# Performance work log

Measured on AMD Instinct MI355X. Metric: run time of the kernel, lower is better.

Reference implementation:

```python
import jax, jax.numpy as jnp
import numpy as np

N_NODES = 50000
N_EDGES = 1_600_000
NFEAT, NHID, NLAYERS, NCLASS = 512, 256, 4, 40


def spmm(edge_src, edge_dst, edge_val, X):
    # sparse adj (COO) @ X : gather rows by src, scale, scatter-add to dst
    msg = X[edge_src] * edge_val[:, None]          # [E, F]
    return jax.ops.segment_sum(msg, edge_dst, num_segments=N_NODES)


def setup_inputs() -> dict:
    key = jax.random.key(0)
    ks = jax.random.split(key, 16)
    x = jax.random.normal(ks[0], (N_NODES, NFEAT), dtype=jnp.float32)
    edge_src = jax.random.randint(ks[1], (N_EDGES,), 0, N_NODES, dtype=jnp.int32)
    edge_dst = jax.random.randint(ks[2], (N_EDGES,), 0, N_NODES, dtype=jnp.int32)
    edge_val = jax.random.uniform(ks[3], (N_EDGES,), dtype=jnp.float32)

    def mk_w(k, fan_in, fan_out):
        return jax.random.normal(k, (fan_in, fan_out), dtype=jnp.float32) / jnp.sqrt(jnp.float32(fan_in))

    inp = {"x": x, "edge_val": edge_val, "edge_src": edge_src, "edge_dst": edge_dst}
    for k in range(NLAYERS):
        fan_in = k * NHID + NFEAT
        inp[f"W{k}"] = mk_w(ks[4 + k], fan_in, NHID)
        inp[f"b{k}"] = jnp.zeros((NHID,), dtype=jnp.float32)
    inp["W_out"] = mk_w(ks[12], NLAYERS * NHID + NFEAT, NCLASS)
    inp["b_out"] = jnp.zeros((NCLASS,), dtype=jnp.float32)
    return inp


def reference(x, edge_val, W0, b0, W1, b1, W2, b2, W3, b3, W_out, b_out, edge_src, edge_dst):
    Ws = [(W0, b0), (W1, b1), (W2, b2), (W3, b3)]
    blocks = [x]
    for W, b in Ws:
        h = jnp.concatenate(blocks, axis=1)                       # [N, k*nhid+nfeat]
        h = spmm(edge_src, edge_dst, edge_val, h @ W) + b          # snowball_layer
        blocks.append(jnp.tanh(h))                                 # dropout no-op (eval)
    h = jnp.concatenate(blocks, axis=1)                            # [N, nlayers*nhid+nfeat]
    out = spmm(edge_src, edge_dst, edge_val, h @ W_out) + b_out    # out layer, eye=False
    return jax.nn.log_softmax(out, axis=1)
```

## Files before the change

### kernel.cpp

```cpp
#include <hip/hip_runtime.h>
#include <hip/hip_bf16.h>
#include <math.h>

#define N_NODES 50000
#define N_EDGES 1600000
#define NFEAT   512
#define NHID    256
#define NCLASS  40
#define HCOLS   1536

typedef __attribute__((ext_vector_type(8))) short bf16x8s;
typedef __attribute__((ext_vector_type(4))) float f32x4;

__device__ __forceinline__ ushort f2bf(float f) {
    uint u = __builtin_bit_cast(uint, f);
    uint r = (u + 0x7fffu + ((u >> 16) & 1u)) >> 16;
    return (ushort)r;
}
__device__ __forceinline__ float bf2f(ushort u) {
    uint t = (uint)u << 16;
    return __builtin_bit_cast(float, t);
}

__global__ __launch_bounds__(256) void copy_x_bf16_kernel(const float4* __restrict__ x4,
                                                          ushort* __restrict__ Hb) {
    const int total = N_NODES * (NFEAT / 4);
    for (int idx = blockIdx.x * blockDim.x + threadIdx.x; idx < total;
         idx += gridDim.x * blockDim.x) {
        int node = idx >> 7;
        int j    = idx & 127;
        float4 v = x4[idx];
        ushort4 o;
        o.x = f2bf(v.x); o.y = f2bf(v.y); o.z = f2bf(v.z); o.w = f2bf(v.w);
        *(ushort4*)&Hb[(size_t)node * HCOLS + j * 4] = o;
    }
}

__global__ __launch_bounds__(256) void convert_weights_kernel(
        const float* __restrict__ W0, const float* __restrict__ W1,
        const float* __restrict__ W2, const float* __restrict__ W3,
        const float* __restrict__ Wout,
        ushort* __restrict__ T0, ushort* __restrict__ T1,
        ushort* __restrict__ T2, ushort* __restrict__ T3,
        ushort* __restrict__ Tout) {
    const int S0 = 512 * 256, S1 = 768 * 256, S2 = 1024 * 256, S3 = 1280 * 256;
    const int S4 = 128 * HCOLS;
    const int total = S0 + S1 + S2 + S3 + S4;
    for (int idx = blockIdx.x * blockDim.x + threadIdx.x; idx < total;
         idx += gridDim.x * blockDim.x) {
        int t = idx;
        if (t < S0) {
            int n = t / 512, k = t - n * 512;
            T0[t] = f2bf(W0[(size_t)k * NHID + n]);
        } else if ((t -= S0) < S1) {
            int n = t / 768, k = t - n * 768;
            T1[t] = f2bf(W1[(size_t)k * NHID + n]);
        } else if ((t -= S1) < S2) {
            int n = t / 1024, k = t - n * 1024;
            T2[t] = f2bf(W2[(size_t)k * NHID + n]);
        } else if ((t -= S2) < S3) {
            int n = t / 1280, k = t - n * 1280;
            T3[t] = f2bf(W3[(size_t)k * NHID + n]);
        } else {
            t -= S3;
            int n = t / HCOLS, k = t - n * HCOLS;
            Tout[t] = (n < NCLASS) ? f2bf(Wout[(size_t)k * NCLASS + n]) : (ushort)0;
        }
    }
}

__global__ __launch_bounds__(256) void hist_kernel(const int* __restrict__ dst,
                                                   int* __restrict__ cnt) {
    int i = blockIdx.x * 256 + threadIdx.x;
    if (i < N_EDGES) atomicAdd(&cnt[dst[i]], 1);
}

__global__ __launch_bounds__(1024) void scan_kernel(const int* __restrict__ cnt,
                                                    int* __restrict__ row_ptr) {
    __shared__ int wsum[16];
    __shared__ int carry_s;
    const int tid = threadIdx.x;
    const int lane = tid & 63;
    const int w = tid >> 6;
    if (tid == 0) { carry_s = 0; row_ptr[0] = 0; }
    __syncthreads();
    for (int base = 0; base < N_NODES; base += 1024) {
        int i = base + tid;
        int v = (i < N_NODES) ? cnt[i] : 0;
        int sc = v;
        #pragma unroll
        for (int off = 1; off < 64; off <<= 1) {
            int t = __shfl_up(sc, off);
            if (lane >= off) sc += t;
        }
        if (lane == 63) wsum[w] = sc;
        __syncthreads();
        if (w == 0 && lane < 16) {
            int t = wsum[lane];
            int s2 = t;
            #pragma unroll
            for (int off = 1; off < 16; off <<= 1) {
                int u = __shfl_up(s2, off);
                if (lane >= off) s2 += u;
            }
            wsum[lane] = s2 - t;
        }
        __syncthreads();
        int incl = sc + wsum[w] + carry_s;
        if (i < N_NODES) row_ptr[i + 1] = incl;
        __syncthreads();
        if (tid == 1023) carry_s = incl;
        __syncthreads();
    }
}

__global__ __launch_bounds__(256) void scatter_kernel(const int* __restrict__ src,
                                                      const int* __restrict__ dst,
                                                      const float* __restrict__ val,
                                                      const int* __restrict__ row_ptr,
                                                      int* __restrict__ cnt,
                                                      uint2* __restrict__ edges) {
    int i = blockIdx.x * 256 + threadIdx.x;
    if (i < N_EDGES) {
        int d   = dst[i];
        int pos = row_ptr[d] + atomicAdd(&cnt[d], 1);
        uint2 p;
        p.x = (uint)src[i];
        p.y = __builtin_bit_cast(uint, val[i]);
        edges[pos] = p;
    }
}

__global__ __launch_bounds__(512) void gemm_bf16_wide(const ushort* __restrict__ A, int lda,
                                                      const ushort* __restrict__ Bt, int ldb,
                                                      ushort* __restrict__ C, int ldc,
                                                      int M, int K) {
    __shared__ short As[128 * 32];
    __shared__ short Bs[256 * 32];
    const int tid  = threadIdx.x;
    const int lane = tid & 63;
    const int wid  = tid >> 6;
    const int wr   = wid >> 2;
    const int wc   = wid & 3;
    const int bm   = blockIdx.x * 128;

    f32x4 acc[4][4] = {};
    const int r0 = tid >> 2, ko = (tid & 3) * 8;

    for (int k0 = 0; k0 < K; k0 += 32) {
        {
            const ushort* g = A + (size_t)(bm + r0) * lda + k0 + ko;
            __builtin_amdgcn_global_load_lds((const __attribute__((address_space(1))) void*)g,
                                             (__attribute__((address_space(3))) void*)&As[tid * 8], 16, 0, 0);
        }
        {
            const ushort* g0 = Bt + (size_t)r0 * ldb + k0 + ko;
            const ushort* g1 = Bt + (size_t)(128 + r0) * ldb + k0 + ko;
            __builtin_amdgcn_global_load_lds((const __attribute__((address_space(1))) void*)g0,
                                             (__attribute__((address_space(3))) void*)&Bs[tid * 8], 16, 0, 0);
            __builtin_amdgcn_global_load_lds((const __attribute__((address_space(1))) void*)g1,
                                             (__attribute__((address_space(3))) void*)&Bs[(tid + 512) * 8], 16, 0, 0);
        }
        __syncthreads();

        const int kg = (lane >> 4) * 8;
        const int rr = lane & 15;
        bf16x8s a[4], b[4];
        #pragma unroll
        for (int i = 0; i < 4; ++i)
            a[i] = *(const bf16x8s*)&As[(wr * 64 + i * 16 + rr) * 32 + kg];
        #pragma unroll
        for (int j = 0; j < 4; ++j)
            b[j] = *(const bf16x8s*)&Bs[(wc * 64 + j * 16 + rr) * 32 + kg];
        #pragma unroll
        for (int i = 0; i < 4; ++i)
            #pragma unroll
            for (int j = 0; j < 4; ++j)
                acc[i][j] = __builtin_amdgcn_mfma_f32_16x16x32_bf16(a[i], b[j], acc[i][j], 0, 0, 0);
        __syncthreads();
    }

    const int rowg = (lane >> 4) * 4;
    const int colg = lane & 15;
    #pragma unroll
    for (int i = 0; i < 4; ++i) {
        #pragma unroll
        for (int j = 0; j < 4; ++j) {
            #pragma unroll
            for (int r = 0; r < 4; ++r) {
                int row = bm + wr * 64 + i * 16 + rowg + r;
                int col = wc * 64 + j * 16 + colg;
                if (row < M) C[(size_t)row * ldc + col] = f2bf(acc[i][j][r]);
            }
        }
    }
}

__global__ __launch_bounds__(256) void gemm_bf16(const ushort* __restrict__ A, int lda,
                                                 const ushort* __restrict__ Bt, int ldb,
                                                 ushort* __restrict__ C, int ldc,
                                                 int M, int K, int Nc) {
    __shared__ short As[128 * 32];
    __shared__ short Bs[128 * 32];
    const int tid  = threadIdx.x;
    const int lane = tid & 63;
    const int wid  = tid >> 6;
    const int wr   = wid >> 1;
    const int wc   = wid & 1;
    const int bm   = blockIdx.x * 128;
    const int bn   = blockIdx.y * 128;

    f32x4 acc[4][4] = {};
    const int r0 = tid >> 2, ko = (tid & 3) * 8;

    for (int k0 = 0; k0 < K; k0 += 32) {
        {
            const ushort* g0 = A + (size_t)(bm + r0) * lda + k0 + ko;
            const ushort* g1 = A + (size_t)(bm + 64 + r0) * lda + k0 + ko;
            __builtin_amdgcn_global_load_lds((const __attribute__((address_space(1))) void*)g0,
                                             (__attribute__((address_space(3))) void*)&As[tid * 8], 16, 0, 0);
            __builtin_amdgcn_global_load_lds((const __attribute__((address_space(1))) void*)g1,
                                             (__attribute__((address_space(3))) void*)&As[(tid + 256) * 8], 16, 0, 0);
        }
        {
            const ushort* g0 = Bt + (size_t)(bn + r0) * ldb + k0 + ko;
            const ushort* g1 = Bt + (size_t)(bn + 64 + r0) * ldb + k0 + ko;
            __builtin_amdgcn_global_load_lds((const __attribute__((address_space(1))) void*)g0,
                                             (__attribute__((address_space(3))) void*)&Bs[tid * 8], 16, 0, 0);
            __builtin_amdgcn_global_load_lds((const __attribute__((address_space(1))) void*)g1,
                                             (__attribute__((address_space(3))) void*)&Bs[(tid + 256) * 8], 16, 0, 0);
        }
        __syncthreads();

        const int kg = (lane >> 4) * 8;
        const int rr = lane & 15;
        bf16x8s a[4], b[4];
        #pragma unroll
        for (int i = 0; i < 4; ++i)
            a[i] = *(const bf16x8s*)&As[(wr * 64 + i * 16 + rr) * 32 + kg];
        #pragma unroll
        for (int j = 0; j < 4; ++j)
            b[j] = *(const bf16x8s*)&Bs[(wc * 64 + j * 16 + rr) * 32 + kg];
        #pragma unroll
        for (int i = 0; i < 4; ++i)
            #pragma unroll
            for (int j = 0; j < 4; ++j)
                acc[i][j] = __builtin_amdgcn_mfma_f32_16x16x32_bf16(a[i], b[j], acc[i][j], 0, 0, 0);
        __syncthreads();
    }

    const int rowg = (lane >> 4) * 4;
    const int colg = lane & 15;
    #pragma unroll
    for (int i = 0; i < 4; ++i) {
        #pragma unroll
        for (int j = 0; j < 4; ++j) {
            #pragma unroll
            for (int r = 0; r < 4; ++r) {
                int row = bm + wr * 64 + i * 16 + rowg + r;
                int col = bn + wc * 64 + j * 16 + colg;
                if (row < M && col < Nc) C[(size_t)row * ldc + col] = f2bf(acc[i][j][r]);
            }
        }
    }
}

__global__ __launch_bounds__(256) void spmm256_tanh_kernel(const int* __restrict__ row_ptr,
                                                           const uint2* __restrict__ edges,
                                                           const ushort* __restrict__ Zb,
                                                           const float* __restrict__ bias,
                                                           ushort* __restrict__ out,
                                                           int out_stride) {
    int node = blockIdx.x * 4 + (threadIdx.x >> 6);
    if (node >= N_NODES) return;
    int lane = threadIdx.x & 63;
    int s = row_ptr[node], e = row_ptr[node + 1];
    const ushort4* Z4 = (const ushort4*)Zb;
    float ax = 0.f, ay = 0.f, az = 0.f, aw = 0.f;
    int i = s;
    for (; i + 16 <= e; i += 16) {
        uint2 ed[16]; ushort4 xv[16];
        #pragma unroll
        for (int u = 0; u < 16; ++u) ed[u] = edges[i + u];
        #pragma unroll
        for (int u = 0; u < 16; ++u) xv[u] = Z4[(size_t)ed[u].x * 64 + lane];
        #pragma unroll
        for (int u = 0; u < 16; ++u) {
            float v = __builtin_bit_cast(float, ed[u].y);
            ax += v * bf2f(xv[u].x); ay += v * bf2f(xv[u].y);
            az += v * bf2f(xv[u].z); aw += v * bf2f(xv[u].w);
        }
    }
    for (; i + 4 <= e; i += 4) {
        uint2 ed[4]; ushort4 xv[4];
        #pragma unroll
        for (int u = 0; u < 4; ++u) ed[u] = edges[i + u];
        #pragma unroll
        for (int u = 0; u < 4; ++u) xv[u] = Z4[(size_t)ed[u].x * 64 + lane];
        #pragma unroll
        for (int u = 0; u < 4; ++u) {
            float v = __builtin_bit_cast(float, ed[u].y);
            ax += v * bf2f(xv[u].x); ay += v * bf2f(xv[u].y);
            az += v * bf2f(xv[u].z); aw += v * bf2f(xv[u].w);
        }
    }
    for (; i < e; ++i) {
        uint2 ed = edges[i];
        float v = __builtin_bit_cast(float, ed.y);
        ushort4 x0 = Z4[(size_t)ed.x * 64 + lane];
        ax += v * bf2f(x0.x); ay += v * bf2f(x0.y);
        az += v * bf2f(x0.z); aw += v * bf2f(x0.w);
    }
    float4 b = ((const float4*)bias)[lane];
    ushort4 o;
    o.x = f2bf(tanhf(ax + b.x)); o.y = f2bf(tanhf(ay + b.y));
    o.z = f2bf(tanhf(az + b.z)); o.w = f2bf(tanhf(aw + b.w));
    *(ushort4*)&out[(size_t)node * out_stride + lane * 4] = o;
}

__global__ __launch_bounds__(256) void spmm_out_lsm_kernel(const int* __restrict__ row_ptr,
                                                           const uint2* __restrict__ edges,
                                                           const ushort* __restrict__ Zb,
                                                           const float* __restrict__ bias,
                                                           float* __restrict__ out) {
    int node = blockIdx.x * 4 + (threadIdx.x >> 6);
    if (node >= N_NODES) return;
    int lane = threadIdx.x & 63;
    int e8 = lane >> 3;
    int cg = lane & 7;
    int s = row_ptr[node], e = row_ptr[node + 1];
    float acc[8] = {};
    int i = s;
    for (; i + 8 <= e; i += 8) {
        uint2 ed = edges[i + e8];
        float v  = __builtin_bit_cast(float, ed.y);
        bf16x8s x = *(const bf16x8s*)&Zb[(size_t)ed.x * 64 + cg * 8];
        #pragma unroll
        for (int u = 0; u < 8; ++u) acc[u] += v * bf2f((ushort)x[u]);
    }
    if (i + e8 < e) {
        uint2 ed = edges[i + e8];
        float v  = __builtin_bit_cast(float, ed.y);
        bf16x8s x = *(const bf16x8s*)&Zb[(size_t)ed.x * 64 + cg * 8];
        #pragma unroll
        for (int u = 0; u < 8; ++u) acc[u] += v * bf2f((ushort)x[u]);
    }
    #pragma unroll
    for (int off = 8; off < 64; off <<= 1)
        #pragma unroll
        for (int u = 0; u < 8; ++u) acc[u] += __shfl_xor(acc[u], off);
    float m = -INFINITY;
    #pragma unroll
    for (int u = 0; u < 8; ++u) {
        int col = cg * 8 + u;
        if (col < NCLASS) { acc[u] += bias[col]; m = fmaxf(m, acc[u]); }
    }
    #pragma unroll
    for (int off = 1; off < 8; off <<= 1) m = fmaxf(m, __shfl_xor(m, off));
    float ss = 0.f;
    #pragma unroll
    for (int u = 0; u < 8; ++u) {
        int col = cg * 8 + u;
        if (col < NCLASS) ss += expf(acc[u] - m);
    }
    #pragma unroll
    for (int off = 1; off < 8; off <<= 1) ss += __shfl_xor(ss, off);
    float lse = logf(ss);
    if (e8 == 0) {
        #pragma unroll
        for (int u = 0; u < 8; ++u) {
            int col = cg * 8 + u;
            if (col < NCLASS) out[(size_t)node * NCLASS + col] = acc[u] - m - lse;
        }
    }
}

extern "C" void kernel_launch(void* const* d_in, const int* in_sizes, int n_in,
                              void* d_out, int out_size, void* d_ws, size_t ws_size,
                              hipStream_t stream) {
    const float* x        = (const float*)d_in[0];
    const float* edge_val = (const float*)d_in[1];
    const int*   edge_src = (const int*)d_in[2];
    const int*   edge_dst = (const int*)d_in[3];
    const float* W[4]     = {(const float*)d_in[4], (const float*)d_in[6],
                             (const float*)d_in[8], (const float*)d_in[10]};
    const float* bvec[4]  = {(const float*)d_in[5], (const float*)d_in[7],
                             (const float*)d_in[9], (const float*)d_in[11]};
    const float* W_out    = (const float*)d_in[12];
    const float* b_out    = (const float*)d_in[13];
    float* out = (float*)d_out;

    char* ws = (char*)d_ws;
    ushort* Hb     = (ushort*)ws;
    ushort* Zb     = (ushort*)(ws + 153600000);
    ushort* Zoutb  = (ushort*)(ws + 179200000);
    ushort* Wt[4]  = {(ushort*)(ws + 185600000),
                      (ushort*)(ws + 185862144),
                      (ushort*)(ws + 186255360),
                      (ushort*)(ws + 186779648)};
    ushort* Wt_out = (ushort*)(ws + 187435008);
    uint2*  edges  = (uint2*) (ws + 187828224);
    int*    row_ptr= (int*)   (ws + 200628224);
    int*    cnt    = (int*)   (ws + 200828228);

    hipMemsetAsync(cnt, 0, N_NODES * sizeof(int), stream);
    hist_kernel<<<(N_EDGES + 255) / 256, 256, 0, stream>>>(edge_dst, cnt);
    scan_kernel<<<1, 1024, 0, stream>>>(cnt, row_ptr);
    hipMemsetAsync(cnt, 0, N_NODES * sizeof(int), stream);
    scatter_kernel<<<(N_EDGES + 255) / 256, 256, 0, stream>>>(
        edge_src, edge_dst, edge_val, row_ptr, cnt, edges);

    convert_weights_kernel<<<2048, 256, 0, stream>>>(W[0], W[1], W[2], W[3], W_out,
                                                     Wt[0], Wt[1], Wt[2], Wt[3], Wt_out);
    copy_x_bf16_kernel<<<4096, 256, 0, stream>>>((const float4*)x, Hb);

    for (int k = 0; k < 4; ++k) {
        int fan_in = NFEAT + k * NHID;
        gemm_bf16_wide<<<(N_NODES + 127) / 128, 512, 0, stream>>>(
            Hb, HCOLS, Wt[k], fan_in, Zb, NHID, N_NODES, fan_in);
        spmm256_tanh_kernel<<<(N_NODES + 3) / 4, 256, 0, stream>>>(
            row_ptr, edges, Zb, bvec[k], Hb + NFEAT + k * NHID, HCOLS);
    }

    {
        dim3 g((N_NODES + 127) / 128, 1);
        gemm_bf16<<<g, 256, 0, stream>>>(Hb, HCOLS, Wt_out, HCOLS, Zoutb, 64,
                                         N_NODES, HCOLS, 64);
        spmm_out_lsm_kernel<<<(N_NODES + 3) / 4, 256, 0, stream>>>(
            row_ptr, edges, Zoutb, b_out, out);
    }
    (void)in_sizes; (void)n_in; (void)out_size; (void)ws_size;
}
```

Baseline: 908.4 us.

## Split hidden-layer SpMM into two 128-column passes for cache locality

The per-layer SpMM over 256 bf16 columns is split into two launches that each process 128 columns. Each lane now loads 4 bytes instead of 8 per edge, so each pass gathers from a 128-column half of Z, about 12.8 MB instead of 25.6 MB, which is more likely to stay resident in L2 or the infinity cache. The cost is reading the edge list and row pointers twice and launching an extra kernel per layer.

```diff
diff --git a/kernel.cpp b/kernel.cpp
--- a/kernel.cpp
+++ b/kernel.cpp
@@ -265,57 +265,61 @@
     }
 }
 
-__global__ __launch_bounds__(256) void spmm256_tanh_kernel(const int* __restrict__ row_ptr,
+__global__ __launch_bounds__(256) void spmm128_tanh_kernel(const int* __restrict__ row_ptr,
                                                            const uint2* __restrict__ edges,
                                                            const ushort* __restrict__ Zb,
                                                            const float* __restrict__ bias,
                                                            ushort* __restrict__ out,
-                                                           int out_stride) {
+                                                           int out_stride, int c0) {
     int node = blockIdx.x * 4 + (threadIdx.x >> 6);
     if (node >= N_NODES) return;
     int lane = threadIdx.x & 63;
     int s = row_ptr[node], e = row_ptr[node + 1];
-    const ushort4* Z4 = (const ushort4*)Zb;
-    float ax = 0.f, ay = 0.f, az = 0.f, aw = 0.f;
+    const uint* Z2 = (const uint*)Zb;
+    const int zoff = (c0 >> 1) + lane;
+    float ax = 0.f, ay = 0.f;
     int i = s;
     for (; i + 16 <= e; i += 16) {
-        uint2 ed[16]; ushort4 xv[16];
+        uint2 ed[16]; uint xv[16];
         #pragma unroll
         for (int u = 0; u < 16; ++u) ed[u] = edges[i + u];
         #pragma unroll
-        for (int u = 0; u < 16; ++u) xv[u] = Z4[(size_t)ed[u].x * 64 + lane];
+        for (int u = 0; u < 16; ++u) xv[u] = Z2[(size_t)ed[u].x * 128 + zoff];
         #pragma unroll
         for (int u = 0; u < 16; ++u) {
-            float v = __builtin_bit_cast(float, ed[u].y);
-            ax += v * bf2f(xv[u].x); ay += v * bf2f(xv[u].y);
-            az += v * bf2f(xv[u].z); aw += v * bf2f(xv[u].w);
+            float v  = __builtin_bit_cast(float, ed[u].y);
+            float xl = __builtin_bit_cast(float, xv[u] << 16);
+            float xh = __builtin_bit_cast(float, xv[u] & 0xffff0000u);
+            ax += v * xl; ay += v * xh;
         }
     }
     for (; i + 4 <= e; i += 4) {
-        uint2 ed[4]; ushort4 xv[4];
+        uint2 ed[4]; uint xv[4];
         #pragma unroll
         for (int u = 0; u < 4; ++u) ed[u] = edges[i + u];
         #pragma unroll
-        for (int u = 0; u < 4; ++u) xv[u] = Z4[(size_t)ed[u].x * 64 + lane];
+        for (int u = 0; u < 4; ++u) xv[u] = Z2[(size_t)ed[u].x * 128 + zoff];
         #pragma unroll
         for (int u = 0; u < 4; ++u) {
-            float v = __builtin_bit_cast(float, ed[u].y);
-            ax += v * bf2f(xv[u].x); ay += v * bf2f(xv[u].y);
-            az += v * bf2f(xv[u].z); aw += v * bf2f(xv[u].w);
+            float v  = __builtin_bit_cast(float, ed[u].y);
+            float xl = __builtin_bit_cast(float, xv[u] << 16);
+            float xh = __builtin_bit_cast(float, xv[u] & 0xffff0000u);
+            ax += v * xl; ay += v * xh;
         }
     }
     for (; i < e; ++i) {
         uint2 ed = edges[i];
-        float v = __builtin_bit_cast(float, ed.y);
-        ushort4 x0 = Z4[(size_t)ed.x * 64 + lane];
-        ax += v * bf2f(x0.x); ay += v * bf2f(x0.y);
-        az += v * bf2f(x0.z); aw += v * bf2f(x0.w);
-    }
-    float4 b = ((const float4*)bias)[lane];
-    ushort4 o;
-    o.x = f2bf(tanhf(ax + b.x)); o.y = f2bf(tanhf(ay + b.y));
-    o.z = f2bf(tanhf(az + b.z)); o.w = f2bf(tanhf(aw + b.w));
-    *(ushort4*)&out[(size_t)node * out_stride + lane * 4] = o;
+        float v  = __builtin_bit_cast(float, ed.y);
+        uint x0  = Z2[(size_t)ed.x * 128 + zoff];
+        float xl = __builtin_bit_cast(float, x0 << 16);
+        float xh = __builtin_bit_cast(float, x0 & 0xffff0000u);
+        ax += v * xl; ay += v * xh;
+    }
+    float2 b = ((const float2*)(bias + c0))[lane];
+    ushort2 o;
+    o.x = f2bf(tanhf(ax + b.x));
+    o.y = f2bf(tanhf(ay + b.y));
+    *(ushort2*)&out[(size_t)node * out_stride + c0 + lane * 2] = o;
 }
 
 __global__ __launch_bounds__(256) void spmm_out_lsm_kernel(const int* __restrict__ row_ptr,
@@ -418,8 +422,10 @@
         int fan_in = NFEAT + k * NHID;
         gemm_bf16_wide<<<(N_NODES + 127) / 128, 512, 0, stream>>>(
             Hb, HCOLS, Wt[k], fan_in, Zb, NHID, N_NODES, fan_in);
-        spmm256_tanh_kernel<<<(N_NODES + 3) / 4, 256, 0, stream>>>(
-            row_ptr, edges, Zb, bvec[k], Hb + NFEAT + k * NHID, HCOLS);
+        spmm128_tanh_kernel<<<(N_NODES + 3) / 4, 256, 0, stream>>>(
+            row_ptr, edges, Zb, bvec[k], Hb + NFEAT + k * NHID, HCOLS, 0);
+        spmm128_tanh_kernel<<<(N_NODES + 3) / 4, 256, 0, stream>>>(
+            row_ptr, edges, Zb, bvec[k], Hb + NFEAT + k * NHID, HCOLS, 128);
     }
 
     {
```

Result: no change. 904.3 us (-0.5%).

## Slice hidden GEMM output into 32-column panels and split SpMM per XCD

Applied to the files above, without the earlier changes.

The hidden-layer GEMM now writes its output as eight column-major panels of 32 columns each, laid out as [slice][node][32]. The SpMM kernel assigns each slice to blockIdx modulo 8. Because consecutive blocks round-robin across the eight XCDs, each XCD touches only one 3.2 MB panel, which should fit in its L2 and improve gather reuse. Within a wave, 8 lanes cover 32 columns and 8 edge groups run in parallel, followed by a shuffle reduction. The cost is eight times more edge-list reads, plus the reduction and reliance on the hardware's block-to-XCD dispatch order.

```diff
diff --git a/kernel.cpp b/kernel.cpp
--- a/kernel.cpp
+++ b/kernel.cpp
@@ -8,6 +8,7 @@
 #define NHID    256
 #define NCLASS  40
 #define HCOLS   1536
+#define SLICE_STRIDE ((size_t)N_NODES * 32)
 
 typedef __attribute__((ext_vector_type(8))) short bf16x8s;
 typedef __attribute__((ext_vector_type(4))) float f32x4;
@@ -133,7 +134,7 @@
 
 __global__ __launch_bounds__(512) void gemm_bf16_wide(const ushort* __restrict__ A, int lda,
                                                       const ushort* __restrict__ Bt, int ldb,
-                                                      ushort* __restrict__ C, int ldc,
+                                                      ushort* __restrict__ C,
                                                       int M, int K) {
     __shared__ short As[128 * 32];
     __shared__ short Bs[256 * 32];
@@ -186,11 +187,13 @@
     for (int i = 0; i < 4; ++i) {
         #pragma unroll
         for (int j = 0; j < 4; ++j) {
+            const int col = wc * 64 + j * 16 + colg;
+            const int cb  = col >> 5, cw = col & 31;
             #pragma unroll
             for (int r = 0; r < 4; ++r) {
                 int row = bm + wr * 64 + i * 16 + rowg + r;
-                int col = wc * 64 + j * 16 + colg;
-                if (row < M) C[(size_t)row * ldc + col] = f2bf(acc[i][j][r]);
+                if (row < M)
+                    C[(size_t)cb * SLICE_STRIDE + (size_t)row * 32 + cw] = f2bf(acc[i][j][r]);
             }
         }
     }
@@ -265,57 +268,73 @@
     }
 }
 
-__global__ __launch_bounds__(256) void spmm256_tanh_kernel(const int* __restrict__ row_ptr,
-                                                           const uint2* __restrict__ edges,
-                                                           const ushort* __restrict__ Zb,
-                                                           const float* __restrict__ bias,
-                                                           ushort* __restrict__ out,
-                                                           int out_stride) {
-    int node = blockIdx.x * 4 + (threadIdx.x >> 6);
+__global__ __launch_bounds__(256) void spmm32_xcd_kernel(const int* __restrict__ row_ptr,
+                                                         const uint2* __restrict__ edges,
+                                                         const ushort* __restrict__ Z,
+                                                         const float* __restrict__ bias,
+                                                         ushort* __restrict__ out,
+                                                         int out_stride) {
+    const int cb   = blockIdx.x & 7;
+    const int node = (blockIdx.x >> 3) * 4 + (threadIdx.x >> 6);
     if (node >= N_NODES) return;
-    int lane = threadIdx.x & 63;
-    int s = row_ptr[node], e = row_ptr[node + 1];
-    const ushort4* Z4 = (const ushort4*)Zb;
-    float ax = 0.f, ay = 0.f, az = 0.f, aw = 0.f;
+    const int lane = threadIdx.x & 63;
+    const int eg   = lane >> 3;
+    const int c    = lane & 7;
+    const int s = row_ptr[node], e = row_ptr[node + 1];
+
+    const ushort* Zs = Z + (size_t)cb * SLICE_STRIDE;
+    const unsigned long long* e8p = (const unsigned long long*)edges;
+    const int zo = c * 4;
+
+    float a0 = 0.f, a1 = 0.f, a2 = 0.f, a3 = 0.f;
     int i = s;
-    for (; i + 16 <= e; i += 16) {
-        uint2 ed[16]; ushort4 xv[16];
-        #pragma unroll
-        for (int u = 0; u < 16; ++u) ed[u] = edges[i + u];
-        #pragma unroll
-        for (int u = 0; u < 16; ++u) xv[u] = Z4[(size_t)ed[u].x * 64 + lane];
-        #pragma unroll
-        for (int u = 0; u < 16; ++u) {
-            float v = __builtin_bit_cast(float, ed[u].y);
-            ax += v * bf2f(xv[u].x); ay += v * bf2f(xv[u].y);
-            az += v * bf2f(xv[u].z); aw += v * bf2f(xv[u].w);
-        }
-    }
-    for (; i + 4 <= e; i += 4) {
-        uint2 ed[4]; ushort4 xv[4];
-        #pragma unroll
-        for (int u = 0; u < 4; ++u) ed[u] = edges[i + u];
-        #pragma unroll
-        for (int u = 0; u < 4; ++u) xv[u] = Z4[(size_t)ed[u].x * 64 + lane];
+    for (; i + 32 <= e; i += 32) {
+        unsigned long long pk[4];
+        uint2 xv[4];
+        #pragma unroll
+        for (int u = 0; u < 4; ++u)
+            pk[u] = __builtin_nontemporal_load(&e8p[i + u * 8 + eg]);
+        #pragma unroll
+        for (int u = 0; u < 4; ++u)
+            xv[u] = *(const uint2*)&Zs[(size_t)(uint)pk[u] * 32 + zo];
         #pragma unroll
         for (int u = 0; u < 4; ++u) {
-            float v = __builtin_bit_cast(float, ed[u].y);
-            ax += v * bf2f(xv[u].x); ay += v * bf2f(xv[u].y);
-            az += v * bf2f(xv[u].z); aw += v * bf2f(xv[u].w);
-        }
-    }
-    for (; i < e; ++i) {
-        uint2 ed = edges[i];
-        float v = __builtin_bit_cast(float, ed.y);
-        ushort4 x0 = Z4[(size_t)ed.x * 64 + lane];
-        ax += v * bf2f(x0.x); ay += v * bf2f(x0.y);
-        az += v * bf2f(x0.z); aw += v * bf2f(x0.w);
-    }
-    float4 b = ((const float4*)bias)[lane];
-    ushort4 o;
-    o.x = f2bf(tanhf(ax + b.x)); o.y = f2bf(tanhf(ay + b.y));
-    o.z = f2bf(tanhf(az + b.z)); o.w = f2bf(tanhf(aw + b.w));
-    *(ushort4*)&out[(size_t)node * out_stride + lane * 4] = o;
+            float v = __builtin_bit_cast(float, (uint)(pk[u] >> 32));
+            a0 += v * __builtin_bit_cast(float, xv[u].x << 16);
+            a1 += v * __builtin_bit_cast(float, xv[u].x & 0xffff0000u);
+            a2 += v * __builtin_bit_cast(float, xv[u].y << 16);
+            a3 += v * __builtin_bit_cast(float, xv[u].y & 0xffff0000u);
+        }
+    }
+    for (; i < e; i += 8) {
+        int j = i + eg;
+        bool act = j < e;
+        int jj = act ? j : (e - 1);
+        unsigned long long pk = __builtin_nontemporal_load(&e8p[jj]);
+        uint2 xv = *(const uint2*)&Zs[(size_t)(uint)pk * 32 + zo];
+        float v = act ? __builtin_bit_cast(float, (uint)(pk >> 32)) : 0.f;
+        a0 += v * __builtin_bit_cast(float, xv.x << 16);
+        a1 += v * __builtin_bit_cast(float, xv.x & 0xffff0000u);
+        a2 += v * __builtin_bit_cast(float, xv.y << 16);
+        a3 += v * __builtin_bit_cast(float, xv.y & 0xffff0000u);
+    }
+    #pragma unroll
+    for (int off = 8; off < 64; off <<= 1) {
+        a0 += __shfl_xor(a0, off);
+        a1 += __shfl_xor(a1, off);
+        a2 += __shfl_xor(a2, off);
+        a3 += __shfl_xor(a3, off);
+    }
+    if (eg == 0) {
+        float4 b = *(const float4*)&bias[cb * 32 + c * 4];
+        ushort4 o;
+        o.x = f2bf(tanhf(a0 + b.x));
+        o.y = f2bf(tanhf(a1 + b.y));
+        o.z = f2bf(tanhf(a2 + b.z));
+        o.w = f2bf(tanhf(a3 + b.w));
+        __builtin_nontemporal_store(__builtin_bit_cast(unsigned long long, o),
+            (unsigned long long*)&out[(size_t)node * out_stride + cb * 32 + c * 4]);
+    }
 }
 
 __global__ __launch_bounds__(256) void spmm_out_lsm_kernel(const int* __restrict__ row_ptr,
@@ -417,8 +436,8 @@
     for (int k = 0; k < 4; ++k) {
         int fan_in = NFEAT + k * NHID;
         gemm_bf16_wide<<<(N_NODES + 127) / 128, 512, 0, stream>>>(
-            Hb, HCOLS, Wt[k], fan_in, Zb, NHID, N_NODES, fan_in);
-        spmm256_tanh_kernel<<<(N_NODES + 3) / 4, 256, 0, stream>>>(
+            Hb, HCOLS, Wt[k], fan_in, Zb, N_NODES, fan_in);
+        spmm32_xcd_kernel<<<8 * 12500, 256, 0, stream>>>(
             row_ptr, edges, Zb, bvec[k], Hb + NFEAT + k * NHID, HCOLS);
     }
 
```

New measurement: 1.469 ms. 61.7% more time.
